# Kernel optimization log

Hardware: AMD Instinct MI355X
Metric: run time of the kernel (lower is better)

The kernel has to match this reference:

```python
import jax, jax.numpy as jnp
import numpy as np

COMMITMENT_COST = 0.25


def setup_inputs() -> dict:
    key = jax.random.key(0)
    k1, k2 = jax.random.split(key)
    x = jax.random.normal(k1, (4, 64, 32, 32, 32), dtype=jnp.float32)
    weight = jax.random.normal(k2, (512, 64), dtype=jnp.float32)
    return {"x": x, "weight": weight}


def reference(x, weight):
    b, c, h, w, d = x.shape  # c == embed_dim
    # [b, h, w, d, c] -> [N, c]
    flat = jnp.transpose(x, (0, 2, 3, 4, 1)).reshape(-1, c)
    # squared L2 distances to each codebook vector: [N, n_embed]
    distances = (
        jnp.sum(flat * flat, axis=1, keepdims=True)
        - 2.0 * (flat @ weight.T)
        + jnp.sum(weight * weight, axis=1)
    )
    embed_idx_flat = jnp.argmin(distances, axis=1)  # == argmax(-distances)
    embed_idx = embed_idx_flat.reshape(b, h, w, d)
    # gather codebook rows and move embed dim back to channel position
    quantized = jnp.transpose(weight[embed_idx], (0, 4, 1, 2, 3))  # [b, c, h, w, d]
    latent_loss = COMMITMENT_COST * jnp.mean(
        (jax.lax.stop_gradient(quantized) - x) ** 2
    )
    quantized_st = jax.lax.stop_gradient(quantized - x) + x
    return quantized_st, embed_idx, latent_loss
```

## Files before the change

### kernel.cpp

```cpp
#include <hip/hip_runtime.h>
#include <hip/hip_bf16.h>

#define HWD      32768
#define NC       64
#define NE       512
#define OUT_IDX  8388608
#define OUT_LOSS 8519680

#define WS_WSQ_F   16
#define WS_SLOT_F  528
#define WS_WP_B    4096
#define WS_NEEDED  200704

typedef __attribute__((ext_vector_type(8))) short bf16x8;
typedef __attribute__((ext_vector_type(4))) float f32x4;

__device__ inline unsigned short bf16_rne(float v) {
    unsigned u = __builtin_bit_cast(unsigned, v);
    return (unsigned short)((u + 0x7FFFu + ((u >> 16) & 1u)) >> 16);
}
__device__ inline float bf16_f(unsigned short s) {
    return __builtin_bit_cast(float, (unsigned)s << 16);
}
__device__ inline void split3(float v, unsigned short& h, unsigned short& m,
                              unsigned short& l) {
    h = bf16_rne(v);
    float r1 = v - bf16_f(h);
    m = bf16_rne(r1);
    float r2 = r1 - bf16_f(m);
    l = bf16_rne(r2);
}

__global__ __launch_bounds__(256) void vq_prep(
    const float* __restrict__ w, float* __restrict__ ws)
{
    const int gtid = blockIdx.x * 256 + threadIdx.x;
    if (gtid == 0) { ws[0] = 0.f; ((unsigned*)ws)[1] = 0u; }
    if (gtid < 256) ws[WS_SLOT_F + gtid] = 0.f;
    if (gtid < NE) {
        const float4* row = (const float4*)(w + (size_t)gtid * NC);
        float s0 = 0.f, s1 = 0.f, s2 = 0.f, s3 = 0.f;
#pragma unroll
        for (int k = 0; k < 16; ++k) {
            float4 v = row[k];
            s0 = fmaf(v.x, v.x, s0); s1 = fmaf(v.y, v.y, s1);
            s2 = fmaf(v.z, v.z, s2); s3 = fmaf(v.w, v.w, s3);
        }
        ws[WS_WSQ_F + gtid] = (s0 + s1) + (s2 + s3);
    }
    const int lane_s = gtid & 63;
    int t = gtid >> 6;
    const int plane = t % 3; t /= 3;
    const int kc = t & 1;
    const int ct = t >> 1;
    const int code = ct * 16 + (lane_s & 15);
    const int kb   = kc * 32 + (lane_s >> 4) * 8;
    const float* src = w + (size_t)code * NC + kb;
    unsigned short o[8];
#pragma unroll
    for (int j = 0; j < 8; ++j) {
        unsigned short h, m, l;
        split3(src[j], h, m, l);
        o[j] = (plane == 0) ? h : (plane == 1) ? m : l;
    }
    unsigned short* dst = (unsigned short*)((char*)ws + WS_WP_B) + (size_t)gtid * 8;
#pragma unroll
    for (int j = 0; j < 8; ++j) dst[j] = o[j];
}

__device__ __forceinline__ void tileUpd(const bf16x8 A[2][2][3],
                                        const bf16x8 B[2][3], const float wsq,
                                        const int ct, const int lanelo,
                                        float best[2][4], int bidx[2][4])
{
#pragma unroll
    for (int pt = 0; pt < 2; ++pt) {
        f32x4 acc = {0.f, 0.f, 0.f, 0.f};
        acc = __builtin_amdgcn_mfma_f32_16x16x32_bf16(A[pt][0][2], B[0][0], acc, 0, 0, 0);
        acc = __builtin_amdgcn_mfma_f32_16x16x32_bf16(A[pt][1][2], B[1][0], acc, 0, 0, 0);
        acc = __builtin_amdgcn_mfma_f32_16x16x32_bf16(A[pt][0][1], B[0][1], acc, 0, 0, 0);
        acc = __builtin_amdgcn_mfma_f32_16x16x32_bf16(A[pt][1][1], B[1][1], acc, 0, 0, 0);
        acc = __builtin_amdgcn_mfma_f32_16x16x32_bf16(A[pt][0][0], B[0][2], acc, 0, 0, 0);
        acc = __builtin_amdgcn_mfma_f32_16x16x32_bf16(A[pt][1][0], B[1][2], acc, 0, 0, 0);
        acc = __builtin_amdgcn_mfma_f32_16x16x32_bf16(A[pt][0][1], B[0][0], acc, 0, 0, 0);
        acc = __builtin_amdgcn_mfma_f32_16x16x32_bf16(A[pt][1][1], B[1][0], acc, 0, 0, 0);
        acc = __builtin_amdgcn_mfma_f32_16x16x32_bf16(A[pt][0][0], B[0][1], acc, 0, 0, 0);
        acc = __builtin_amdgcn_mfma_f32_16x16x32_bf16(A[pt][1][0], B[1][1], acc, 0, 0, 0);
        acc = __builtin_amdgcn_mfma_f32_16x16x32_bf16(A[pt][0][0], B[0][0], acc, 0, 0, 0);
        acc = __builtin_amdgcn_mfma_f32_16x16x32_bf16(A[pt][1][0], B[1][0], acc, 0, 0, 0);
#pragma unroll
        for (int r = 0; r < 4; ++r) {
            const float d = fmaf(-2.f, acc[r], wsq);
            if (d < best[pt][r]) { best[pt][r] = d; bidx[pt][r] = ct * 16 + lanelo; }
        }
    }
}

__global__ __launch_bounds__(256, 4) void vq_argmin(
    const float* __restrict__ x, float* __restrict__ ws,
    float* __restrict__ out)
{
    __shared__ int   idx_sh[128];
    __shared__ __align__(16) char Bsh[2][6144];
    __shared__ float wsq_sh[NE];

    const int tid    = threadIdx.x;
    const int wv     = tid >> 6;
    const int lane   = tid & 63;
    const int lanelo = lane & 15;
    const int quad   = lane >> 4;
    const int posB   = blockIdx.x * 128;
    const int b      = posB >> 15;
    const int hwdB   = posB & (HWD - 1);
    const size_t xoff = (size_t)b * NC * HWD + hwdB;
    const int wpos   = wv * 32;

    const char*  wpB  = (const char*)ws + WS_WP_B;
    const float* wsqp = ws + WS_WSQ_F;

    auto stageB = [&](int t, int bsel) {
#pragma unroll
        for (int cc = 0; cc < 2; ++cc) {
            const int c = wv + 4 * cc;
            if (c < 6) {
                const char* g = wpB + ((size_t)(t * 6 + c) * 64 + lane) * 16;
                void* l = &Bsh[bsel][c * 1024];
                __builtin_amdgcn_global_load_lds(
                    (const __attribute__((address_space(1))) unsigned*)g,
                    (__attribute__((address_space(3))) unsigned*)l, 16, 0, 0);
            }
        }
    };

    stageB(0, 0);
    { wsq_sh[tid] = wsqp[tid]; wsq_sh[tid + 256] = wsqp[tid + 256]; }

    bf16x8 A[2][2][3];
#pragma unroll
    for (int pt = 0; pt < 2; ++pt) {
#pragma unroll
        for (int kc = 0; kc < 2; ++kc) {
            bf16x8 fh, fm, fl;
#pragma unroll
            for (int j = 0; j < 8; ++j) {
                const int k = kc * 32 + quad * 8 + j;
                const float v = x[xoff + (size_t)k * HWD + wpos + pt * 16 + lanelo];
                unsigned short h, m, l;
                split3(v, h, m, l);
                fh[j] = (short)h; fm[j] = (short)m; fl[j] = (short)l;
            }
            A[pt][kc][0] = fh; A[pt][kc][1] = fm; A[pt][kc][2] = fl;
        }
    }

    float best[2][4];
    int   bidx[2][4];
#pragma unroll
    for (int pt = 0; pt < 2; ++pt)
#pragma unroll
        for (int r = 0; r < 4; ++r) { best[pt][r] = 3.402823466e38f; bidx[pt][r] = 0; }

    __syncthreads();

#pragma unroll 1
    for (int t = 0; t < 32; ++t) {
        const int cur = t & 1;
        if (t < 31) stageB(t + 1, cur ^ 1);
        bf16x8 B[2][3];
        const bf16x8* bb = (const bf16x8*)Bsh[cur];
#pragma unroll
        for (int kc = 0; kc < 2; ++kc)
#pragma unroll
            for (int p = 0; p < 3; ++p)
                B[kc][p] = bb[(kc * 3 + p) * 64 + lane];
        const float wsq_c = wsq_sh[t * 16 + lanelo];
        tileUpd(A, B, wsq_c, t, lanelo, best, bidx);
        __syncthreads();
    }

#pragma unroll
    for (int pt = 0; pt < 2; ++pt)
#pragma unroll
        for (int r = 0; r < 4; ++r) {
            float d = best[pt][r]; int i = bidx[pt][r];
#pragma unroll
            for (int mlane = 1; mlane <= 8; mlane <<= 1) {
                const float d2 = __shfl_xor(d, mlane);
                const int   i2 = __shfl_xor(i, mlane);
                if (d2 < d || (d2 == d && i2 < i)) { d = d2; i = i2; }
            }
            if (lanelo == 0)
                idx_sh[wpos + pt * 16 + quad * 4 + r] = i;
        }
    __syncthreads();

    if (tid < 128) out[OUT_IDX + posB + tid] = (float)idx_sh[tid];
}

__global__ __launch_bounds__(256, 8) void vq_epilogue(
    const float* __restrict__ x, const float* __restrict__ w,
    float* __restrict__ ws, float* __restrict__ out)
{
    __shared__ float q_sh[64 * 65];
    __shared__ int   idx_sh[64];
    __shared__ float wred[4];

    const int tid  = threadIdx.x;
    const int posB = blockIdx.x * 64;
    const int b    = posB >> 15;
    const int hwdB = posB & (HWD - 1);
    const size_t xoff = (size_t)b * NC * HWD + hwdB;

    if (tid < 64) idx_sh[tid] = (int)out[OUT_IDX + posB + tid];
    __syncthreads();

#pragma unroll
    for (int it = 0; it < 16; ++it) {
        const int e = it * 256 + tid;
        const int r = e >> 6, c = e & 63;
        q_sh[r * 65 + c] = w[(size_t)idx_sh[r] * NC + c];
    }
    __syncthreads();

    float lsum = 0.f;
#pragma unroll
    for (int it = 0; it < 16; ++it) {
        const int e = it * 256 + tid;
        const int c = e >> 6;
        const int p = e & 63;
        const size_t off = xoff + (size_t)c * HWD + p;
        const float xv = x[off];
        const float q  = q_sh[p * 65 + c];
        const float dq = q - xv;
        lsum = fmaf(dq, dq, lsum);
        out[off] = dq + xv;
    }

#pragma unroll
    for (int off = 32; off >= 1; off >>= 1) lsum += __shfl_down(lsum, off);
    if ((tid & 63) == 0) wred[tid >> 6] = lsum;
    __syncthreads();
    if (tid == 0)
        atomicAdd(ws + WS_SLOT_F + (blockIdx.x & 255),
                  (wred[0] + wred[1]) + (wred[2] + wred[3]));
}

__global__ __launch_bounds__(64) void vq_loss_fin(
    const float* __restrict__ ws, float* __restrict__ out)
{
    const int lane = threadIdx.x;
    float s = (ws[WS_SLOT_F + lane]       + ws[WS_SLOT_F + lane + 64]) +
              (ws[WS_SLOT_F + lane + 128] + ws[WS_SLOT_F + lane + 192]);
#pragma unroll
    for (int off = 32; off >= 1; off >>= 1) s += __shfl_down(s, off);
    if (lane == 0) out[OUT_LOSS] = 0.25f * s / 8388608.0f;
}

__global__ __launch_bounds__(256, 2) void vq_fused_fb(
    const float* __restrict__ x, const float* __restrict__ w,
    float* __restrict__ out, float* __restrict__ loss_acc)
{
    __shared__ float lw[256 * NC];
    __shared__ float wsq[256];
    __shared__ float wred[4];
    const int tid = threadIdx.x;
    const int n0  = blockIdx.x * 512;
    const int b   = n0 >> 15;
    const int hwd = (n0 & (HWD - 1)) + tid;
    const float* xp = x + (size_t)b * NC * HWD + hwd;
    float xr0[NC], xr1[NC];
#pragma unroll
    for (int c = 0; c < NC; ++c) { xr0[c] = xp[(size_t)c * HWD]; xr1[c] = xp[(size_t)c * HWD + 256]; }
    float xsq0 = 0.f, xsq1 = 0.f;
#pragma unroll
    for (int c = 0; c < NC; ++c) { xsq0 = fmaf(xr0[c], xr0[c], xsq0); xsq1 = fmaf(xr1[c], xr1[c], xsq1); }
    float best0 = 3.402823466e38f, best1 = 3.402823466e38f;
    int bi0 = 0, bi1 = 0;
    for (int pass = 0; pass < 2; ++pass) {
        if (pass) __syncthreads();
        const float4* wt = (const float4*)(w + pass * 256 * NC);
        float4* l4 = (float4*)lw;
#pragma unroll
        for (int k = 0; k < 16; ++k) l4[tid + k * 256] = wt[tid + k * 256];
        {
            const float4* row = wt + tid * 16;
            float s0 = 0.f, s1 = 0.f, s2 = 0.f, s3 = 0.f;
#pragma unroll
            for (int k = 0; k < 16; ++k) {
                float4 v = row[k];
                s0 = fmaf(v.x, v.x, s0); s1 = fmaf(v.y, v.y, s1);
                s2 = fmaf(v.z, v.z, s2); s3 = fmaf(v.w, v.w, s3);
            }
            wsq[tid] = (s0 + s1) + (s2 + s3);
        }
        __syncthreads();
#pragma unroll 2
        for (int e = 0; e < 256; ++e) {
            const float4* row = (const float4*)(lw + e * NC);
            float a0 = 0.f, a1 = 0.f, c0 = 0.f, c1 = 0.f;
#pragma unroll
            for (int k = 0; k < 16; ++k) {
                float4 v = row[k];
                a0 = fmaf(xr0[4 * k + 0], v.x, a0); a1 = fmaf(xr0[4 * k + 1], v.y, a1);
                a0 = fmaf(xr0[4 * k + 2], v.z, a0); a1 = fmaf(xr0[4 * k + 3], v.w, a1);
                c0 = fmaf(xr1[4 * k + 0], v.x, c0); c1 = fmaf(xr1[4 * k + 1], v.y, c1);
                c0 = fmaf(xr1[4 * k + 2], v.z, c0); c1 = fmaf(xr1[4 * k + 3], v.w, c1);
            }
            const float d0 = (xsq0 - 2.f * (a0 + a1)) + wsq[e];
            const float d1 = (xsq1 - 2.f * (c0 + c1)) + wsq[e];
            const int ge = pass * 256 + e;
            if (d0 < best0) { best0 = d0; bi0 = ge; }
            if (d1 < best1) { best1 = d1; bi1 = ge; }
        }
    }
    float* o0 = out + (size_t)b * NC * HWD + hwd;
    float lsum = 0.f;
    const float4* r0 = (const float4*)(w + bi0 * NC);
    const float4* r1 = (const float4*)(w + bi1 * NC);
#pragma unroll
    for (int k = 0; k < 16; ++k) {
        float4 q0 = r0[k], q1 = r1[k];
        float qv0[4] = { q0.x, q0.y, q0.z, q0.w };
        float qv1[4] = { q1.x, q1.y, q1.z, q1.w };
#pragma unroll
        for (int j = 0; j < 4; ++j) {
            const int c = 4 * k + j;
            const float dv0 = qv0[j] - xr0[c];
            const float dv1 = qv1[j] - xr1[c];
            lsum = fmaf(dv0, dv0, lsum); lsum = fmaf(dv1, dv1, lsum);
            o0[(size_t)c * HWD] = dv0 + xr0[c];
            o0[(size_t)c * HWD + 256] = dv1 + xr1[c];
        }
    }
    const int n = b * HWD + hwd;
    out[OUT_IDX + n] = (float)bi0;
    out[OUT_IDX + n + 256] = (float)bi1;
#pragma unroll
    for (int off = 32; off >= 1; off >>= 1) lsum += __shfl_down(lsum, off);
    if ((tid & 63) == 0) wred[tid >> 6] = lsum;
    __syncthreads();
    if (tid == 0) atomicAdd(loss_acc, (wred[0] + wred[1]) + (wred[2] + wred[3]));
}

__global__ void vq_loss_fin_fb(const float* __restrict__ acc, float* __restrict__ out)
{
    out[OUT_LOSS] = 0.25f * acc[0] / 8388608.0f;
}

extern "C" void kernel_launch(void* const* d_in, const int* in_sizes, int n_in,
                              void* d_out, int out_size, void* d_ws, size_t ws_size,
                              hipStream_t stream)
{
    const float* x = (const float*)d_in[0];
    const float* w = (const float*)d_in[1];
    float* out = (float*)d_out;
    float* ws  = (float*)d_ws;

    if (ws_size >= WS_NEEDED) {
        vq_prep<<<48, 256, 0, stream>>>(w, ws);
        vq_argmin<<<1024, 256, 0, stream>>>(x, ws, out);
        vq_epilogue<<<2048, 256, 0, stream>>>(x, w, ws, out);
        vq_loss_fin<<<1, 64, 0, stream>>>(ws, out);
    } else {
        hipMemsetAsync(d_ws, 0, sizeof(float), stream);
        vq_fused_fb<<<256, 256, 0, stream>>>(x, w, out, ws);
        vq_loss_fin_fb<<<1, 1, 0, stream>>>(ws, out);
    }
}
```

Measured before the change: 135.9 us.

## Process two codebook tiles per barrier and vectorize epilogue with float4

The argmin kernel grows the LDS codebook staging from a double buffer to four slots and processes two tiles between barriers, halving the number of __syncthreads and prefetching two tiles ahead. Separately, the epilogue stores gathered codebook rows transposed in shared memory so each thread can load x and write the output with float4 accesses. The cost is more LDS per block, which may reduce occupancy for the argmin kernel, and the summation order of the loss changes slightly.

Result: no change. 135.6 us (-0.2%).

```diff
diff --git a/kernel.cpp b/kernel.cpp
--- a/kernel.cpp
+++ b/kernel.cpp
@@ -101,7 +101,7 @@
     float* __restrict__ out)
 {
     __shared__ int   idx_sh[128];
-    __shared__ __align__(16) char Bsh[2][6144];
+    __shared__ __align__(16) char Bsh[4][6144];
     __shared__ float wsq_sh[NE];
 
     const int tid    = threadIdx.x;
@@ -133,6 +133,7 @@
     };
 
     stageB(0, 0);
+    stageB(1, 1);
     { wsq_sh[tid] = wsqp[tid]; wsq_sh[tid + 256] = wsqp[tid + 256]; }
 
     bf16x8 A[2][2][3];
@@ -163,18 +164,25 @@
     __syncthreads();
 
 #pragma unroll 1
-    for (int t = 0; t < 32; ++t) {
-        const int cur = t & 1;
-        if (t < 31) stageB(t + 1, cur ^ 1);
-        bf16x8 B[2][3];
-        const bf16x8* bb = (const bf16x8*)Bsh[cur];
-#pragma unroll
-        for (int kc = 0; kc < 2; ++kc)
-#pragma unroll
-            for (int p = 0; p < 3; ++p)
-                B[kc][p] = bb[(kc * 3 + p) * 64 + lane];
-        const float wsq_c = wsq_sh[t * 16 + lanelo];
-        tileUpd(A, B, wsq_c, t, lanelo, best, bidx);
+    for (int r = 0; r < 16; ++r) {
+        const int base = (r & 1) * 2;
+        if (r < 15) {
+            stageB(2 * r + 2, base ^ 2);
+            stageB(2 * r + 3, (base ^ 2) + 1);
+        }
+#pragma unroll
+        for (int s = 0; s < 2; ++s) {
+            const int t = 2 * r + s;
+            bf16x8 B[2][3];
+            const bf16x8* bb = (const bf16x8*)Bsh[base + s];
+#pragma unroll
+            for (int kc = 0; kc < 2; ++kc)
+#pragma unroll
+                for (int p = 0; p < 3; ++p)
+                    B[kc][p] = bb[(kc * 3 + p) * 64 + lane];
+            const float wsq_c = wsq_sh[t * 16 + lanelo];
+            tileUpd(A, B, wsq_c, t, lanelo, best, bidx);
+        }
         __syncthreads();
     }
 
@@ -201,7 +209,7 @@
     const float* __restrict__ x, const float* __restrict__ w,
     float* __restrict__ ws, float* __restrict__ out)
 {
-    __shared__ float q_sh[64 * 65];
+    __shared__ float q_t[64 * 68];
     __shared__ int   idx_sh[64];
     __shared__ float wred[4];
 
@@ -218,22 +226,27 @@
     for (int it = 0; it < 16; ++it) {
         const int e = it * 256 + tid;
         const int r = e >> 6, c = e & 63;
-        q_sh[r * 65 + c] = w[(size_t)idx_sh[r] * NC + c];
+        q_t[c * 68 + r] = w[(size_t)idx_sh[r] * NC + c];
     }
     __syncthreads();
 
     float lsum = 0.f;
 #pragma unroll
-    for (int it = 0; it < 16; ++it) {
-        const int e = it * 256 + tid;
-        const int c = e >> 6;
-        const int p = e & 63;
-        const size_t off = xoff + (size_t)c * HWD + p;
-        const float xv = x[off];
-        const float q  = q_sh[p * 65 + c];
-        const float dq = q - xv;
-        lsum = fmaf(dq, dq, lsum);
-        out[off] = dq + xv;
+    for (int it = 0; it < 4; ++it) {
+        const int s  = it * 256 + tid;
+        const int c  = s >> 4;
+        const int p0 = (s & 15) * 4;
+        const size_t off = xoff + (size_t)c * HWD + p0;
+        const float4 xv = *(const float4*)(x + off);
+        const float4 qv = *(const float4*)(q_t + c * 68 + p0);
+        const float dx = qv.x - xv.x, dy = qv.y - xv.y;
+        const float dz = qv.z - xv.z, dw = qv.w - xv.w;
+        lsum = fmaf(dx, dx, lsum); lsum = fmaf(dy, dy, lsum);
+        lsum = fmaf(dz, dz, lsum); lsum = fmaf(dw, dw, lsum);
+        float4 ov;
+        ov.x = dx + xv.x; ov.y = dy + xv.y;
+        ov.z = dz + xv.z; ov.w = dw + xv.w;
+        *(float4*)(out + off) = ov;
     }
 
 #pragma unroll
```
